# Kernel tuning notes

Measured on AMD Instinct MI355X. Metric: run time of the kernel, lower is better.

The kernel has to match this reference:

```python
import jax, jax.numpy as jnp
import numpy as np

NUM_EXPERTS = 8
EMBED_DIM = 1024
BATCH, SEQ = 4, 2048


def setup_inputs() -> dict:
    key = jax.random.key(0)
    k1, k2, k3 = jax.random.split(key, 3)
    E_symb = jax.random.normal(k1, (BATCH, SEQ, EMBED_DIM), dtype=jnp.float32)
    gate_w = jax.random.normal(k2, (EMBED_DIM, NUM_EXPERTS), dtype=jnp.float32) * 0.02
    gate_b = jnp.zeros((NUM_EXPERTS,), dtype=jnp.float32)
    expert_w = jax.random.normal(k3, (NUM_EXPERTS, EMBED_DIM, EMBED_DIM), dtype=jnp.float32) * 0.02
    return {"E_symb": E_symb, "gate_w": gate_w, "gate_b": gate_b,
            "expert_w": expert_w, "k": 2}


def reference(E_symb, gate_w, gate_b, expert_w, k):
    B, S, D = E_symb.shape
    E = expert_w.shape[0]
    x = E_symb.reshape(-1, D)                       # [T, D]
    logits = x @ gate_w + gate_b                    # [T, E]
    probs = jax.nn.softmax(logits.astype(jnp.float32), axis=-1)
    # top-k selection; NOTE: original renormalizes routing_weights but never
    # applies them to expert outputs -> combine is an UNWEIGHTED sum.
    _, sel = jax.lax.top_k(probs, k)                # [T, k]
    mask = jax.nn.one_hot(sel, E, dtype=x.dtype).sum(axis=1)  # [T, E] in {0,1}
    # dense grouped-GEMM then masked combine (replaces per-expert gather/scatter loop)
    y = jnp.einsum('td,edf->tef', x, expert_w)      # [T, E, D]
    out = jnp.einsum('tef,te->tf', y, mask)         # [T, D]
    return out.reshape(B, S, D)
```

## Files before the change

kernel.cpp:

```cpp
#include <hip/hip_runtime.h>
#include <hip/hip_bf16.h>
#include <stdint.h>

#define T_TOK 8192
#define DIM   1024
#define NEXP  8
#define BM    128
#define BN    128
#define BK2   32

typedef __bf16 bf16_t;
typedef bf16_t bf16x8 __attribute__((ext_vector_type(8)));
typedef bf16_t bf16x4 __attribute__((ext_vector_type(4)));
typedef float  f32x4  __attribute__((ext_vector_type(4)));

#define WS_CNT    0
#define CIDX(p)   ((p) << 4)
#define WS_LIST   8192
#define WS_XBF    (4u << 20)
#define WS_WT     (20u << 20)

__device__ __forceinline__ void gload16(const void* g, void* l) {
    __builtin_amdgcn_global_load_lds(
        (const __attribute__((address_space(1))) unsigned int*)g,
        (__attribute__((address_space(3))) unsigned int*)l, 16, 0, 0);
}

__device__ __forceinline__ int swz32(int r, int k) {
    return ((r * BK2 + k) * 2) ^ (((r >> 1) & 3) << 4);
}

#define WAITCNT_VM0()   do { asm volatile("s_waitcnt vmcnt(0)" ::: "memory"); \
                             __builtin_amdgcn_sched_barrier(0); } while (0)
#define WAITCNT_VM6()   do { asm volatile("s_waitcnt vmcnt(6)" ::: "memory"); \
                             __builtin_amdgcn_sched_barrier(0); } while (0)
#define BARRIER()       do { __builtin_amdgcn_s_barrier(); \
                             __builtin_amdgcn_sched_barrier(0); } while (0)

__global__ void zero_cnt(int4* cnt4) {
    cnt4[threadIdx.x] = int4{0, 0, 0, 0};
}

__global__ __launch_bounds__(256) void pre1(const float* __restrict__ x,
                                            const float* __restrict__ gw,
                                            const float* __restrict__ gb,
                                            const float* __restrict__ ew,
                                            bf16_t* __restrict__ xbf,
                                            bf16_t* __restrict__ wt,
                                            int* __restrict__ cnt,
                                            int* __restrict__ list) {
    __shared__ __align__(16) float sh[NEXP * DIM];
    int bx  = blockIdx.x;
    int tid = threadIdx.x;
    if (bx < 1024) {
        float4 gb0 = *(const float4*)gb;
        float4 gb1 = *(const float4*)(gb + 4);
        float gbl[8] = {gb0.x, gb0.y, gb0.z, gb0.w, gb1.x, gb1.y, gb1.z, gb1.w};
        float* gwt = sh;
        const float4* gw4 = (const float4*)gw;
        #pragma unroll
        for (int i = 0; i < 8; i++) {
            int f4 = tid + i * 256;
            float4 v = gw4[f4];
            int d  = f4 >> 1;
            int e0 = (f4 & 1) * 4;
            gwt[(e0 + 0) * DIM + d] = v.x;
            gwt[(e0 + 1) * DIM + d] = v.y;
            gwt[(e0 + 2) * DIM + d] = v.z;
            gwt[(e0 + 3) * DIM + d] = v.w;
        }
        __syncthreads();
        int wid  = tid >> 6;
        int lane = tid & 63;
        const float4* gwt4 = (const float4*)gwt;
        for (int tt = 0; tt < 2; tt++) {
            int t = bx * 8 + wid * 2 + tt;
            const float4* xr4 = (const float4*)(x + (size_t)t * DIM);
            float acc[NEXP] = {};
            #pragma unroll
            for (int j = 0; j < 4; j++) {
                int c4 = j * 64 + lane;
                float4 v = xr4[c4];
                bf16x4 b;
                b[0] = (bf16_t)v.x; b[1] = (bf16_t)v.y;
                b[2] = (bf16_t)v.z; b[3] = (bf16_t)v.w;
                *(bf16x4*)(xbf + (size_t)t * DIM + c4 * 4) = b;
                #pragma unroll
                for (int e = 0; e < NEXP; e++) {
                    float4 g = gwt4[e * 256 + c4];
                    acc[e] += v.x * g.x + v.y * g.y + v.z * g.z + v.w * g.w;
                }
            }
            for (int off = 32; off >= 1; off >>= 1)
                #pragma unroll
                for (int e = 0; e < NEXP; e++)
                    acc[e] += __shfl_xor(acc[e], off, 64);
            if (lane == 0) {
                float logit[NEXP];
                #pragma unroll
                for (int e = 0; e < NEXP; e++) logit[e] = acc[e] + gbl[e];
                int b1 = 0; float best = logit[0];
                for (int e = 1; e < NEXP; e++) if (logit[e] > best) { best = logit[e]; b1 = e; }
                int b2 = -1; float best2 = -3.0e38f;
                for (int e = 0; e < NEXP; e++) {
                    if (e == b1) continue;
                    if (logit[e] > best2) { best2 = logit[e]; b2 = e; }
                }
                int a = min(b1, b2), bb = max(b1, b2);
                int p = a * 8 + bb;
                int pos = atomicAdd(&cnt[CIDX(p)], 1);
                list[p * T_TOK + pos] = t;
            }
        }
    } else {
        int bz  = bx - 1024;
        int g   = bz >> 8;
        int rem = bz & 255;
        int f0  = (rem & 15) * 64;
        int d0  = (rem >> 4) * 64;
        float (*tile)[65] = (float (*)[65])sh;
        const float* s1 = ew + ((size_t)g * DIM + d0) * DIM + f0;
        int fl = (tid & 15) * 4;
        int dl = tid >> 4;
        #pragma unroll
        for (int i = 0; i < 4; i++) {
            int d = dl + i * 16;
            float4 u = *(const float4*)(s1 + (size_t)d * DIM + fl);
            tile[d][fl + 0] = u.x; tile[d][fl + 1] = u.y;
            tile[d][fl + 2] = u.z; tile[d][fl + 3] = u.w;
        }
        __syncthreads();
        bf16_t* dst = wt + ((size_t)g * DIM + f0) * DIM + d0;
        int dl2 = (tid & 7) * 8;
        int fl2 = tid >> 3;
        #pragma unroll
        for (int i = 0; i < 2; i++) {
            int f = fl2 + i * 32;
            bf16x8 o;
            #pragma unroll
            for (int c = 0; c < 8; c++) o[c] = (bf16_t)tile[dl2 + c][f];
            *(bf16x8*)(dst + (size_t)f * DIM + dl2) = o;
        }
    }
}

__global__ __launch_bounds__(256, 3) void moe_gemm2(const bf16_t* __restrict__ xbf,
                                                    const bf16_t* __restrict__ wt,
                                                    const int* __restrict__ cnt,
                                                    const int* __restrict__ list,
                                                    float* __restrict__ out) {
    __shared__ __align__(16) bf16_t As[2][BM * BK2];
    __shared__ __align__(16) bf16_t B1[2][BN * BK2];
    __shared__ __align__(16) bf16_t B2[2][BN * BK2];
    __shared__ int toks[BM];
    __shared__ int s_desc[128];
    __shared__ int s_ntile;
    int tid  = threadIdx.x;
    int lane = tid & 63;
    int wv   = tid >> 6;
    int wm   = wv >> 1, wn = wv & 1;

    if (tid < 64) {
        int c  = cnt[CIDX(tid)];
        int tp = (c + BM - 1) >> 7;
        int pre = 0, tot = 0;
        for (int i = 0; i < 64; i++) {
            int v = __shfl(tp, i, 64);
            if (i < tid) pre += v;
            tot += v;
        }
        for (int j = 0; j < tp; j++)
            s_desc[pre + j] = tid | ((j * BM) << 8);
        if (tid == 0) s_ntile = tot;
    }
    __syncthreads();
    int nwork = s_ntile * (DIM / BN);
    int q = nwork >> 3, r = nwork & 7;
    int xcd  = blockIdx.x & 7;
    int slot = blockIdx.x >> 3;
    int share = q + (xcd < r ? 1 : 0);
    if (slot >= share) return;
    int w = xcd * q + min(xcd, r) + slot;

    int dsc = s_desc[w >> 3];
    int n0  = (w & 7) * BN;
    int p   = dsc & 63;
    int m0  = dsc >> 8;
    int e1  = p >> 3, e2 = p & 7;
    int cp  = cnt[CIDX(p)];
    int valid = min(BM, cp - m0);
    if (tid < BM) toks[tid] = list[p * T_TOK + m0 + min(tid, valid - 1)];
    __syncthreads();

    const bf16_t *asrc[2], *b1src[2], *b2src[2];
    const bf16_t* w1 = wt + (size_t)e1 * DIM * DIM;
    const bf16_t* w2 = wt + (size_t)e2 * DIM * DIM;
    #pragma unroll
    for (int i = 0; i < 2; i++) {
        int c = i * 256 + tid;
        int rr = c >> 2, js = (c & 3) ^ ((rr >> 1) & 3);
        asrc[i]  = xbf + (size_t)toks[rr] * DIM + js * 8;
        b1src[i] = w1 + (size_t)(n0 + rr) * DIM + js * 8;
        b2src[i] = w2 + (size_t)(n0 + rr) * DIM + js * 8;
    }

    f32x4 acc[4][4] = {};
    int lr = lane & 15;
    int lk = (lane >> 4) * 8;

    #pragma unroll
    for (int i = 0; i < 2; i++) {
        int lds = (i * 256 + wv * 64) * 8;
        gload16(asrc[i],  &As[0][lds]);
        gload16(b1src[i], &B1[0][lds]);
        gload16(b2src[i], &B2[0][lds]);
    }

    for (int ks = 0; ks < DIM / BK2; ks++) {
        int cur = ks & 1;
        if (ks < DIM / BK2 - 1) {
            int k1 = (ks + 1) * BK2;
            #pragma unroll
            for (int i = 0; i < 2; i++) {
                int lds = (i * 256 + wv * 64) * 8;
                gload16(asrc[i] + k1,  &As[cur ^ 1][lds]);
                gload16(b1src[i] + k1, &B1[cur ^ 1][lds]);
                gload16(b2src[i] + k1, &B2[cur ^ 1][lds]);
            }
            WAITCNT_VM6();
        } else {
            WAITCNT_VM0();
        }
        BARRIER();
        const char* Ab  = (const char*)As[cur];
        const char* B1b = (const char*)B1[cur];
        const char* B2b = (const char*)B2[cur];
        bf16x8 af[4], b1f[4], b2f[4];
        #pragma unroll
        for (int mf = 0; mf < 4; mf++)
            af[mf] = *(const bf16x8*)(Ab + swz32(wm * 64 + mf * 16 + lr, lk));
        #pragma unroll
        for (int nf = 0; nf < 4; nf++) {
            b1f[nf] = *(const bf16x8*)(B1b + swz32(wn * 64 + nf * 16 + lr, lk));
            b2f[nf] = *(const bf16x8*)(B2b + swz32(wn * 64 + nf * 16 + lr, lk));
        }
        #pragma unroll
        for (int mf = 0; mf < 4; mf++)
            #pragma unroll
            for (int nf = 0; nf < 4; nf++)
                acc[mf][nf] = __builtin_amdgcn_mfma_f32_16x16x32_bf16(
                    af[mf], b1f[nf], acc[mf][nf], 0, 0, 0);
        #pragma unroll
        for (int mf = 0; mf < 4; mf++)
            #pragma unroll
            for (int nf = 0; nf < 4; nf++)
                acc[mf][nf] = __builtin_amdgcn_mfma_f32_16x16x32_bf16(
                    af[mf], b2f[nf], acc[mf][nf], 0, 0, 0);
        BARRIER();
    }

    #pragma unroll
    for (int mf = 0; mf < 4; mf++) {
        #pragma unroll
        for (int reg = 0; reg < 4; reg++) {
            int rl = wm * 64 + mf * 16 + (lane >> 4) * 4 + reg;
            if (rl < valid) {
                size_t trow = (size_t)toks[rl] * DIM;
                #pragma unroll
                for (int nf = 0; nf < 4; nf++)
                    out[trow + n0 + wn * 64 + nf * 16 + lr] = acc[mf][nf][reg];
            }
        }
    }
}

extern "C" void kernel_launch(void* const* d_in, const int* in_sizes, int n_in,
                              void* d_out, int out_size, void* d_ws, size_t ws_size,
                              hipStream_t stream) {
    const float* x  = (const float*)d_in[0];
    const float* gw = (const float*)d_in[1];
    const float* gb = (const float*)d_in[2];
    const float* ew = (const float*)d_in[3];
    float* out = (float*)d_out;
    char* ws = (char*)d_ws;
    int*    cnt  = (int*)(ws + WS_CNT);
    int*    list = (int*)(ws + WS_LIST);
    bf16_t* xbf  = (bf16_t*)(ws + WS_XBF);
    bf16_t* wt   = (bf16_t*)(ws + WS_WT);

    zero_cnt<<<dim3(1), 256, 0, stream>>>((int4*)cnt);
    pre1<<<dim3(3072), 256, 0, stream>>>(x, gw, gb, ew, xbf, wt, cnt, list);
    moe_gemm2<<<dim3(1024), 256, 0, stream>>>(xbf, wt, cnt, list, out);
}
```

Measured before the change: 77.71 us.

## Sum the two expert weight tiles on the fly so each tile needs one GEMM

```diff
diff --git a/kernel.cpp b/kernel.cpp
--- a/kernel.cpp
+++ b/kernel.cpp
@@ -20,6 +20,9 @@
 #define WS_XBF    (4u << 20)
 #define WS_WT     (20u << 20)
 
+__device__ const int d_PA[28] = {0,0,0,0,0,0,0,1,1,1,1,1,1,2,2,2,2,2,3,3,3,3,4,4,4,5,5,6};
+__device__ const int d_PB[28] = {1,2,3,4,5,6,7,2,3,4,5,6,7,3,4,5,6,7,4,5,6,7,5,6,7,6,7,7};
+
 __device__ __forceinline__ void gload16(const void* g, void* l) {
     __builtin_amdgcn_global_load_lds(
         (const __attribute__((address_space(1))) unsigned int*)g,
@@ -33,6 +36,8 @@
 #define WAITCNT_VM0()   do { asm volatile("s_waitcnt vmcnt(0)" ::: "memory"); \
                              __builtin_amdgcn_sched_barrier(0); } while (0)
 #define WAITCNT_VM6()   do { asm volatile("s_waitcnt vmcnt(6)" ::: "memory"); \
+                             __builtin_amdgcn_sched_barrier(0); } while (0)
+#define WAITCNT_LGKM0() do { asm volatile("s_waitcnt lgkmcnt(0)" ::: "memory"); \
                              __builtin_amdgcn_sched_barrier(0); } while (0)
 #define BARRIER()       do { __builtin_amdgcn_s_barrier(); \
                              __builtin_amdgcn_sched_barrier(0); } while (0)
@@ -144,14 +149,13 @@
     }
 }
 
-__global__ __launch_bounds__(256, 3) void moe_gemm2(const bf16_t* __restrict__ xbf,
+__global__ __launch_bounds__(256, 4) void moe_gemm3(const bf16_t* __restrict__ xbf,
                                                     const bf16_t* __restrict__ wt,
                                                     const int* __restrict__ cnt,
                                                     const int* __restrict__ list,
                                                     float* __restrict__ out) {
     __shared__ __align__(16) bf16_t As[2][BM * BK2];
-    __shared__ __align__(16) bf16_t B1[2][BN * BK2];
-    __shared__ __align__(16) bf16_t B2[2][BN * BK2];
+    __shared__ __align__(16) bf16_t Bs[2][BN * BK2];
     __shared__ int toks[BM];
     __shared__ int s_desc[128];
     __shared__ int s_ntile;
@@ -192,70 +196,79 @@
     if (tid < BM) toks[tid] = list[p * T_TOK + m0 + min(tid, valid - 1)];
     __syncthreads();
 
-    const bf16_t *asrc[2], *b1src[2], *b2src[2];
-    const bf16_t* w1 = wt + (size_t)e1 * DIM * DIM;
-    const bf16_t* w2 = wt + (size_t)e2 * DIM * DIM;
+    const bf16_t* asrc[2];
     #pragma unroll
     for (int i = 0; i < 2; i++) {
         int c = i * 256 + tid;
         int rr = c >> 2, js = (c & 3) ^ ((rr >> 1) & 3);
-        asrc[i]  = xbf + (size_t)toks[rr] * DIM + js * 8;
-        b1src[i] = w1 + (size_t)(n0 + rr) * DIM + js * 8;
-        b2src[i] = w2 + (size_t)(n0 + rr) * DIM + js * 8;
+        asrc[i] = xbf + (size_t)toks[rr] * DIM + js * 8;
+    }
+    const bf16_t* w1 = wt + (size_t)e1 * DIM * DIM;
+    const bf16_t* w2 = wt + (size_t)e2 * DIM * DIM;
+    const bf16_t* b1p[2];
+    const bf16_t* b2p[2];
+    int bofs[2];
+    #pragma unroll
+    for (int i = 0; i < 2; i++) {
+        int c = i * 256 + tid;
+        int f = c >> 2, j = c & 3;
+        b1p[i] = w1 + (size_t)(n0 + f) * DIM + j * 8;
+        b2p[i] = w2 + (size_t)(n0 + f) * DIM + j * 8;
+        bofs[i] = swz32(f, j * 8);
     }
 
     f32x4 acc[4][4] = {};
     int lr = lane & 15;
     int lk = (lane >> 4) * 8;
 
-    #pragma unroll
-    for (int i = 0; i < 2; i++) {
-        int lds = (i * 256 + wv * 64) * 8;
-        gload16(asrc[i],  &As[0][lds]);
-        gload16(b1src[i], &B1[0][lds]);
-        gload16(b2src[i], &B2[0][lds]);
-    }
+    bf16x8 br1[2], br2[2];
+    #pragma unroll
+    for (int i = 0; i < 2; i++) { br1[i] = *(const bf16x8*)b1p[i];
+                                  br2[i] = *(const bf16x8*)b2p[i]; }
+    #pragma unroll
+    for (int i = 0; i < 2; i++)
+        gload16(asrc[i], &As[0][(i * 256 + wv * 64) * 8]);
 
     for (int ks = 0; ks < DIM / BK2; ks++) {
         int cur = ks & 1;
+        #pragma unroll
+        for (int i = 0; i < 2; i++) {
+            bf16x8 o;
+            #pragma unroll
+            for (int qq = 0; qq < 8; qq++)
+                o[qq] = (bf16_t)((float)br1[i][qq] + (float)br2[i][qq]);
+            *(bf16x8*)((char*)Bs[cur] + bofs[i]) = o;
+        }
         if (ks < DIM / BK2 - 1) {
             int k1 = (ks + 1) * BK2;
             #pragma unroll
-            for (int i = 0; i < 2; i++) {
-                int lds = (i * 256 + wv * 64) * 8;
-                gload16(asrc[i] + k1,  &As[cur ^ 1][lds]);
-                gload16(b1src[i] + k1, &B1[cur ^ 1][lds]);
-                gload16(b2src[i] + k1, &B2[cur ^ 1][lds]);
-            }
+            for (int i = 0; i < 2; i++) { br1[i] = *(const bf16x8*)(b1p[i] + k1);
+                                          br2[i] = *(const bf16x8*)(b2p[i] + k1); }
+            #pragma unroll
+            for (int i = 0; i < 2; i++)
+                gload16(asrc[i] + k1, &As[cur ^ 1][(i * 256 + wv * 64) * 8]);
+            WAITCNT_LGKM0();
             WAITCNT_VM6();
         } else {
+            WAITCNT_LGKM0();
             WAITCNT_VM0();
         }
         BARRIER();
-        const char* Ab  = (const char*)As[cur];
-        const char* B1b = (const char*)B1[cur];
-        const char* B2b = (const char*)B2[cur];
-        bf16x8 af[4], b1f[4], b2f[4];
+        const char* Ab = (const char*)As[cur];
+        const char* Bb = (const char*)Bs[cur];
+        bf16x8 af[4], bfr[4];
         #pragma unroll
         for (int mf = 0; mf < 4; mf++)
             af[mf] = *(const bf16x8*)(Ab + swz32(wm * 64 + mf * 16 + lr, lk));
         #pragma unroll
-        for (int nf = 0; nf < 4; nf++) {
-            b1f[nf] = *(const bf16x8*)(B1b + swz32(wn * 64 + nf * 16 + lr, lk));
-            b2f[nf] = *(const bf16x8*)(B2b + swz32(wn * 64 + nf * 16 + lr, lk));
-        }
+        for (int nf = 0; nf < 4; nf++)
+            bfr[nf] = *(const bf16x8*)(Bb + swz32(wn * 64 + nf * 16 + lr, lk));
         #pragma unroll
         for (int mf = 0; mf < 4; mf++)
             #pragma unroll
             for (int nf = 0; nf < 4; nf++)
                 acc[mf][nf] = __builtin_amdgcn_mfma_f32_16x16x32_bf16(
-                    af[mf], b1f[nf], acc[mf][nf], 0, 0, 0);
-        #pragma unroll
-        for (int mf = 0; mf < 4; mf++)
-            #pragma unroll
-            for (int nf = 0; nf < 4; nf++)
-                acc[mf][nf] = __builtin_amdgcn_mfma_f32_16x16x32_bf16(
-                    af[mf], b2f[nf], acc[mf][nf], 0, 0, 0);
+                    af[mf], bfr[nf], acc[mf][nf], 0, 0, 0);
         BARRIER();
     }
 
@@ -290,5 +303,5 @@
 
     zero_cnt<<<dim3(1), 256, 0, stream>>>((int4*)cnt);
     pre1<<<dim3(3072), 256, 0, stream>>>(x, gw, gb, ew, xbf, wt, cnt, list);
-    moe_gemm2<<<dim3(1024), 256, 0, stream>>>(xbf, wt, cnt, list, out);
-}
+    moe_gemm3<<<dim3(1024), 256, 0, stream>>>(xbf, wt, cnt, list, out);
+}
```

Result: faster. 71.78 us (-7.6%).
